# Optimization experiments

Measured on AMD Instinct MI355X. Metric: run time of the kernel, lower is better.

## Reference

```python
import jax, jax.numpy as jnp
import numpy as np

D_STATE = 16
DT_RANK = 6
EPS = 1e-5


def layer_norm(x, w, b):
    mu = jnp.mean(x, axis=-1, keepdims=True)
    var = jnp.mean((x - mu) ** 2, axis=-1, keepdims=True)
    return (x - mu) * jax.lax.rsqrt(var + EPS) * w + b


def selective_scan(u, delta, A, Bp, Cp, Dp):
    # u, delta: [B,L,D]; A: [D,N]; Bp, Cp: [B,L,N]; Dp: [D]
    delta_A = jnp.exp(jnp.einsum('bld,dn->bldn', delta, A))          # [B,L,D,N]
    delta_B_u = jnp.einsum('bld,bln,bld->bldn', delta, Bp, u)        # [B,L,D,N]
    Bsz, L, D = u.shape

    def step(x, inp):
        dA_t, dBu_t, C_t = inp                                       # [B,D,N],[B,D,N],[B,N]
        x = dA_t * x + dBu_t
        y = jnp.einsum('bdn,bn->bd', x, C_t)
        return x, y

    x0 = jnp.zeros((Bsz, D, D_STATE), dtype=u.dtype)
    xs = (jnp.swapaxes(delta_A, 0, 1), jnp.swapaxes(delta_B_u, 0, 1), jnp.swapaxes(Cp, 0, 1))
    _, ys = jax.lax.scan(step, x0, xs)                               # ys: [L,B,D]
    y = jnp.swapaxes(ys, 0, 1)
    return y + u * Dp


def ssm(x, x_proj_W, dt_proj_W, dt_proj_b, A_log, D_param):
    A = -jnp.exp(A_log.astype(jnp.float32))                         # [D,N]
    dbc = x @ x_proj_W.T                                             # [B,L,dt_rank+2N]
    delta_r = dbc[..., :DT_RANK]
    Bp = dbc[..., DT_RANK:DT_RANK + D_STATE]
    Cp = dbc[..., DT_RANK + D_STATE:]
    delta = jax.nn.softplus(delta_r @ dt_proj_W.T + dt_proj_b) * 0.001
    return selective_scan(x, delta, A, Bp, Cp, D_param.astype(jnp.float32))


def reference(feat_patch, ln_w, ln_b, in_proj_W, conv_w, conv_b,
              x_proj_W, dt_proj_W, dt_proj_b, A_log, D_param, out_proj_W):
    residual = feat_patch
    x = layer_norm(feat_patch, ln_w, ln_b)
    x = x @ in_proj_W.T                                              # [B,L,96]
    x_ncl = jnp.swapaxes(x, 1, 2)                                    # [B,96,L]
    x_ncl = jax.lax.conv_general_dilated(
        x_ncl, conv_w, window_strides=(1,), padding=((1, 1),),
        dimension_numbers=('NCH', 'OIH', 'NCH'), feature_group_count=96)
    x_ncl = x_ncl + conv_b[None, :, None]
    x = jnp.swapaxes(x_ncl, 1, 2)                                    # [B,L,96]
    x = jax.nn.silu(x)
    y = ssm(x, x_proj_W, dt_proj_W, dt_proj_b, A_log, D_param)
    out = y @ out_proj_W.T                                           # [B,L,2048]
    return out + residual


def setup_inputs() -> dict:
    key = jax.random.key(0)
    ks = jax.random.split(key, 10)
    B, L, C, Din = 16, 2048, 2048, 96
    A = jnp.tile(jnp.arange(1, D_STATE + 1, dtype=jnp.float32)[None, :], (Din, 1))
    return {
        'feat_patch': jax.random.normal(ks[0], (B, L, C), dtype=jnp.float32),
        'ln_w': jnp.ones((C,), jnp.float32),
        'ln_b': jnp.zeros((C,), jnp.float32),
        'in_proj_W': jax.random.normal(ks[1], (Din, C), jnp.float32) * (1.0 / np.sqrt(C)),
        'conv_w': jax.random.normal(ks[2], (Din, 1, 3), jnp.float32) * 0.3,
        'conv_b': jnp.zeros((Din,), jnp.float32),
        'x_proj_W': jax.random.normal(ks[3], (DT_RANK + 2 * D_STATE, Din), jnp.float32) * (1.0 / np.sqrt(Din)),
        'dt_proj_W': jax.random.normal(ks[4], (Din, DT_RANK), jnp.float32) * (1.0 / np.sqrt(DT_RANK)),
        'dt_proj_b': jnp.zeros((Din,), jnp.float32),
        'A_log': jnp.log(A),
        'D_param': jnp.ones((Din,), jnp.float32),
        'out_proj_W': jax.random.normal(ks[5], (C, Din), jnp.float32) * (1.0 / np.sqrt(Din)),
    }
```

## Files before the change

kernel.cpp:

```cpp
#include <hip/hip_runtime.h>
#include <hip/hip_bf16.h>

#define BSZ 16
#define LEN 2048
#define CH  2048
#define DIN 96
#define NST 16
#define RNK 6
#define NROW (BSZ*LEN)
#define TCH  256
#define NCHK (LEN/TCH)
#define NPAIR (BSZ*DIN)

typedef __attribute__((ext_vector_type(4))) float f32x4;
typedef __attribute__((ext_vector_type(8))) short bf16x8;

static __device__ __forceinline__ unsigned short f2bf(float f) {
  union { float f; unsigned u; } v; v.f = f;
  unsigned r = v.u + 0x7fff + ((v.u >> 16) & 1);
  return (unsigned short)(r >> 16);
}

static __device__ __forceinline__ f32x4 mfma16(bf16x8 a, bf16x8 b, f32x4 c) {
  return __builtin_amdgcn_mfma_f32_16x16x32_bf16(a, b, c, 0, 0, 0);
}

__global__ void k_prep(const float* __restrict__ inW, const float* __restrict__ outW,
                       const float* __restrict__ xW, const float* __restrict__ dtW,
                       const float* __restrict__ lnw,
                       unsigned short* __restrict__ inWb, unsigned short* __restrict__ outWb,
                       float* __restrict__ M1t, float* __restrict__ xBC) {
  int i = blockIdx.x * 256 + threadIdx.x;
  if (i < DIN*CH)  inWb[i]  = f2bf(inW[i] * lnw[i & (CH-1)]);
  if (i < CH*DIN)  outWb[i] = f2bf(outW[i]);
  if (i < DIN*DIN) {
    int c = i / DIN, d = i - c*DIN;
    float s = 0.f;
    #pragma unroll
    for (int r = 0; r < RNK; ++r) s += dtW[d*RNK + r] * xW[r*DIN + c];
    M1t[i] = s;
  }
  if (i < DIN*32) {
    int c = i / 32, n = i - c*32;
    xBC[i] = xW[(RNK + n)*DIN + c];
  }
}

__launch_bounds__(256)
__global__ void k_prep2(const float* __restrict__ inW, const float* __restrict__ lnw,
                        const float* __restrict__ lnb,
                        float* __restrict__ pvec, float* __restrict__ qvec) {
  __shared__ float sp_[4], sq_[4];
  const int d = blockIdx.x;
  const int tid = threadIdx.x;
  const float4* w4 = (const float4*)(inW + (size_t)d*CH);
  const float4* a4 = (const float4*)lnw;
  const float4* b4 = (const float4*)lnb;
  float sp = 0.f, sq = 0.f;
  for (int j = tid; j < CH/4; j += 256) {
    float4 w = w4[j], a = a4[j], b = b4[j];
    sp += w.x*a.x + w.y*a.y + w.z*a.z + w.w*a.w;
    sq += w.x*b.x + w.y*b.y + w.z*b.z + w.w*b.w;
  }
  #pragma unroll
  for (int off = 32; off; off >>= 1) { sp += __shfl_xor(sp, off); sq += __shfl_xor(sq, off); }
  if ((tid & 63) == 0) { sp_[tid>>6] = sp; sq_[tid>>6] = sq; }
  __syncthreads();
  if (tid == 0) {
    pvec[d] = sp_[0] + sp_[1] + sp_[2] + sp_[3];
    qvec[d] = sq_[0] + sq_[1] + sq_[2] + sq_[3];
  }
}

#define K2_KC 128
#define K2_WLD 136

__launch_bounds__(512)
__global__ void k_ln_inproj(const float* __restrict__ feat,
                            const unsigned short* __restrict__ Wb,
                            const float* __restrict__ pvec, const float* __restrict__ qvec,
                            float* __restrict__ xin) {
  __shared__ unsigned short W_lds[DIN][K2_WLD];

  const int tid  = threadIdx.x;
  const int lane = tid & 63;
  const int w    = tid >> 6;
  const int wh   = w & 3;
  const int wc   = w >> 2;
  const int r    = lane & 15;
  const int g    = lane >> 4;
  const int row  = blockIdx.x * 64 + wh*16 + r;

  const float* arow = feat + (size_t)row * CH;

  f32x4 acc[3];
  #pragma unroll
  for (int i = 0; i < 3; ++i) acc[i] = (f32x4){0.f, 0.f, 0.f, 0.f};
  float s = 0.f, q = 0.f;

  for (int kc = 0; kc < CH; kc += K2_KC) {
    __syncthreads();
    #pragma unroll
    for (int i = 0; i < 3; ++i) {
      int j = tid + 512*i;
      int wr = j >> 4, c16 = j & 15;
      *(uint4*)&W_lds[wr][c16*8] = *(const uint4*)(Wb + (size_t)wr*CH + kc + c16*8);
    }
    __syncthreads();
    #pragma unroll
    for (int t = 0; t < 4; ++t) {
      const float* ap = arow + kc + t*32 + g*8;
      float4 v0 = *(const float4*)ap;
      float4 v1 = *(const float4*)(ap + 4);
      s += v0.x + v0.y + v0.z + v0.w + v1.x + v1.y + v1.z + v1.w;
      q = fmaf(v0.x, v0.x, q); q = fmaf(v0.y, v0.y, q);
      q = fmaf(v0.z, v0.z, q); q = fmaf(v0.w, v0.w, q);
      q = fmaf(v1.x, v1.x, q); q = fmaf(v1.y, v1.y, q);
      q = fmaf(v1.z, v1.z, q); q = fmaf(v1.w, v1.w, q);
      union { bf16x8 v; unsigned short u[8]; } af;
      af.u[0] = f2bf(v0.x); af.u[1] = f2bf(v0.y); af.u[2] = f2bf(v0.z); af.u[3] = f2bf(v0.w);
      af.u[4] = f2bf(v1.x); af.u[5] = f2bf(v1.y); af.u[6] = f2bf(v1.z); af.u[7] = f2bf(v1.w);
      const int krd = t*32 + g*8;
      #pragma unroll
      for (int ct = 0; ct < 3; ++ct) {
        bf16x8 wf = *(const bf16x8*)&W_lds[wc*48 + ct*16 + r][krd];
        acc[ct] = mfma16(wf, af.v, acc[ct]);
      }
    }
  }

  s += __shfl_xor(s, 16); s += __shfl_xor(s, 32);
  q += __shfl_xor(q, 16); q += __shfl_xor(q, 32);
  const float mu = s * (1.f/CH);
  const float rs = rsqrtf(q*(1.f/CH) - mu*mu + 1e-5f);

  float* orow = xin + (size_t)row * DIN;
  #pragma unroll
  for (int ct = 0; ct < 3; ++ct) {
    const int col = wc*48 + ct*16 + g*4;
    float4 pv = *(const float4*)(pvec + col);
    float4 qv = *(const float4*)(qvec + col);
    f32x4 a = acc[ct];
    float4 o;
    o.x = rs*a[0] - rs*mu*pv.x + qv.x;
    o.y = rs*a[1] - rs*mu*pv.y + qv.y;
    o.z = rs*a[2] - rs*mu*pv.z + qv.z;
    o.w = rs*a[3] - rs*mu*pv.w + qv.w;
    *(float4*)(orow + col) = o;
  }
}

#define K3_R 8
__launch_bounds__(128)
__global__ void k_conv_proj(const float* __restrict__ xin,
                            const float* __restrict__ cw, const float* __restrict__ cb,
                            const float* __restrict__ xBC, const float* __restrict__ M1t,
                            const float* __restrict__ dtb,
                            float* __restrict__ ugT, float* __restrict__ dgT,
                            float* __restrict__ Bg, float* __restrict__ Cg) {
  __shared__ float su[K3_R][DIN];
  const int b  = blockIdx.y;
  const int l0 = blockIdx.x * K3_R;
  const int t  = threadIdx.x;

  if (t < DIN) {
    float x[K3_R + 2];
    #pragma unroll
    for (int i = 0; i < K3_R + 2; ++i) {
      int li = l0 - 1 + i;
      x[i] = (li >= 0 && li < LEN) ? xin[((size_t)b*LEN + li)*DIN + t] : 0.f;
    }
    float w0 = cw[t*3], w1 = cw[t*3+1], w2 = cw[t*3+2], bb = cb[t];
    float ua[K3_R];
    #pragma unroll
    for (int r = 0; r < K3_R; ++r) {
      float c = w0*x[r] + w1*x[r+1] + w2*x[r+2] + bb;
      float uu = c / (1.f + __expf(-c));
      su[r][t] = uu;
      ua[r] = uu;
    }
    float* up = ugT + ((size_t)(b*DIN + t))*LEN + l0;
    *(float4*)(up)     = make_float4(ua[0], ua[1], ua[2], ua[3]);
    *(float4*)(up + 4) = make_float4(ua[4], ua[5], ua[6], ua[7]);
  }
  __syncthreads();
  if (t < DIN) {
    float z[K3_R];
    #pragma unroll
    for (int r = 0; r < K3_R; ++r) z[r] = dtb[t];
    for (int c = 0; c < DIN; ++c) {
      float m = M1t[c*DIN + t];
      #pragma unroll
      for (int r = 0; r < K3_R; ++r) z[r] += su[r][c] * m;
    }
    float da[K3_R];
    #pragma unroll
    for (int r = 0; r < K3_R; ++r) {
      float zz = z[r];
      float sp = (zz > 20.f) ? zz : log1pf(__expf(zz));
      da[r] = 0.001f * sp;
    }
    float* dp = dgT + ((size_t)(b*DIN + t))*LEN + l0;
    *(float4*)(dp)     = make_float4(da[0], da[1], da[2], da[3]);
    *(float4*)(dp + 4) = make_float4(da[4], da[5], da[6], da[7]);
  } else if (t < DIN + 32) {
    int n = t - DIN;
    float s[K3_R];
    #pragma unroll
    for (int r = 0; r < K3_R; ++r) s[r] = 0.f;
    for (int c = 0; c < DIN; ++c) {
      float wv = xBC[c*32 + n];
      #pragma unroll
      for (int r = 0; r < K3_R; ++r) s[r] += su[r][c] * wv;
    }
    #pragma unroll
    for (int r = 0; r < K3_R; ++r) {
      size_t row = (size_t)b*LEN + l0 + r;
      if (n < 16) Bg[row*NST + n]        = s[r];
      else        Cg[row*NST + (n - 16)] = s[r];
    }
  }
}

__launch_bounds__(256)
__global__ void k_scan1(const float* __restrict__ dgT, const float* __restrict__ ugT,
                        const float* __restrict__ Bg, const float* __restrict__ Alog,
                        float* __restrict__ carryS, float* __restrict__ carryD) {
  const int tid  = threadIdx.x;
  const int n    = tid & 15;
  const int pair = blockIdx.x * 16 + (tid >> 4);
  const int chunk = blockIdx.y;
  const int b = pair / DIN, d = pair - b*DIN;
  const float An = -__expf(Alog[d*NST + n]);
  const float* dp  = dgT + ((size_t)(b*DIN + d))*LEN + chunk*TCH;
  const float* up  = ugT + ((size_t)(b*DIN + d))*LEN + chunk*TCH;
  const float* bp_ = Bg + ((size_t)b*LEN + chunk*TCH)*NST + n;

  float s = 0.f, sdl = 0.f;
  #pragma unroll 2
  for (int tq = 0; tq < TCH/4; ++tq) {
    f32x4 dl4 = *(const f32x4*)(dp + tq*4);
    f32x4 uu4 = *(const f32x4*)(up + tq*4);
    #pragma unroll
    for (int j = 0; j < 4; ++j) {
      float dl = dl4[j];
      float bp = bp_[(size_t)(tq*4 + j)*NST];
      s = fmaf(__expf(dl*An), s, dl*bp*uu4[j]);
      sdl += dl;
    }
  }
  carryS[(size_t)(pair*NCHK + chunk)*16 + n] = s;
  if (n == 0) carryD[pair*NCHK + chunk] = sdl;
}

__launch_bounds__(256)
__global__ void k_scan2(const float* __restrict__ carryS, const float* __restrict__ carryD,
                        const float* __restrict__ Alog, float* __restrict__ xstart) {
  const int i = blockIdx.x * 256 + threadIdx.x;
  const int pair = i >> 4, n = i & 15;
  const int d = pair % DIN;
  const float An = -__expf(Alog[d*NST + n]);
  float x = 0.f;
  #pragma unroll
  for (int c = 0; c < NCHK; ++c) {
    xstart[(size_t)(pair*NCHK + c)*16 + n] = x;
    x = fmaf(__expf(An * carryD[pair*NCHK + c]), x, carryS[(size_t)(pair*NCHK + c)*16 + n]);
  }
}

__launch_bounds__(256)
__global__ void k_scan3(const float* __restrict__ dgT, const float* __restrict__ ugT,
                        const float* __restrict__ Bg, const float* __restrict__ Cg,
                        const float* __restrict__ Alog, const float* __restrict__ Dp,
                        const float* __restrict__ xstart, unsigned short* __restrict__ yb) {
  const int tid  = threadIdx.x;
  const int n    = tid & 15;
  const int pair = blockIdx.x * 16 + (tid >> 4);
  const int chunk = blockIdx.y;
  const int b = pair / DIN, d = pair - b*DIN;
  const float An = -__expf(Alog[d*NST + n]);
  const float Dd = Dp[d];
  const float* dp  = dgT + ((size_t)(b*DIN + d))*LEN + chunk*TCH;
  const float* up  = ugT + ((size_t)(b*DIN + d))*LEN + chunk*TCH;
  const float* bp_ = Bg + ((size_t)b*LEN + chunk*TCH)*NST + n;
  const float* cp_ = Cg + ((size_t)b*LEN + chunk*TCH)*NST + n;
  unsigned short* yp = yb + ((size_t)b*LEN + chunk*TCH)*DIN + d;

  float s = xstart[(size_t)(pair*NCHK + chunk)*16 + n];
  #pragma unroll 2
  for (int tq = 0; tq < TCH/4; ++tq) {
    f32x4 dl4 = *(const f32x4*)(dp + tq*4);
    f32x4 uu4 = *(const f32x4*)(up + tq*4);
    #pragma unroll
    for (int j = 0; j < 4; ++j) {
      float dl = dl4[j];
      float bp = bp_[(size_t)(tq*4 + j)*NST];
      float cp = cp_[(size_t)(tq*4 + j)*NST];
      s = fmaf(__expf(dl*An), s, dl*bp*uu4[j]);
      float py = s * cp;
      py += __shfl_xor(py, 8);
      py += __shfl_xor(py, 4);
      py += __shfl_xor(py, 2);
      py += __shfl_xor(py, 1);
      if (n == 0) yp[(size_t)(tq*4 + j)*DIN] = f2bf(py + uu4[j]*Dd);
    }
  }
}

#define K6_MR 128
#define K6_NC 128
#define K6_LD 104

__launch_bounds__(512)
__global__ void k_outproj(const unsigned short* __restrict__ yb,
                          const unsigned short* __restrict__ Wb,
                          const float* __restrict__ resid,
                          float* __restrict__ out) {
  __shared__ unsigned short W_lds[K6_NC][K6_LD];
  const int tid  = threadIdx.x;
  const int lane = tid & 63;
  const int w    = tid >> 6;
  const int r    = lane & 15;
  const int g    = lane >> 4;
  const int r0   = blockIdx.y * K6_MR;
  const int c0   = blockIdx.x * K6_NC;

  #pragma unroll
  for (int i = 0; i < 3; ++i) {
    int j = tid + 512*i;
    int row = j / 12, c8 = j - row*12;
    *(uint4*)&W_lds[row][c8*8] = *(const uint4*)(Wb + (size_t)(c0 + row)*DIN + c8*8);
  }
  __syncthreads();

  f32x4 acc[8];
  #pragma unroll
  for (int i = 0; i < 8; ++i) acc[i] = (f32x4){0.f, 0.f, 0.f, 0.f};

  const unsigned short* yrow = yb + (size_t)(r0 + w*16 + r)*DIN;
  #pragma unroll
  for (int kt = 0; kt < 3; ++kt) {
    const int krd = kt*32 + g*8;
    bf16x8 y0 = *(const bf16x8*)(yrow + krd);
    #pragma unroll
    for (int ci = 0; ci < 8; ++ci) {
      bf16x8 wf = *(const bf16x8*)&W_lds[ci*16 + r][krd];
      acc[ci] = mfma16(wf, y0, acc[ci]);
    }
  }

  const size_t row = (size_t)(r0 + w*16 + r);
  #pragma unroll
  for (int ci = 0; ci < 8; ++ci) {
    size_t col = (size_t)(c0 + ci*16 + g*4);
    const f32x4 rv = *(const f32x4*)(resid + row*CH + col);
    f32x4 o = acc[ci] + rv;
    __builtin_nontemporal_store(o, (f32x4*)(out + row*CH + col));
  }
}

extern "C" void kernel_launch(void* const* d_in, const int* in_sizes, int n_in,
                              void* d_out, int out_size, void* d_ws, size_t ws_size,
                              hipStream_t stream) {
  const float* feat = (const float*)d_in[0];
  const float* lnw  = (const float*)d_in[1];
  const float* lnb  = (const float*)d_in[2];
  const float* inW  = (const float*)d_in[3];
  const float* cw   = (const float*)d_in[4];
  const float* cb   = (const float*)d_in[5];
  const float* xW   = (const float*)d_in[6];
  const float* dtW  = (const float*)d_in[7];
  const float* dtb  = (const float*)d_in[8];
  const float* Alog = (const float*)d_in[9];
  const float* Dp   = (const float*)d_in[10];
  const float* outW = (const float*)d_in[11];
  float* out = (float*)d_out;

  char* ws = (char*)d_ws;
  size_t off = 0;
  auto alloc = [&](size_t bytes) { void* p = ws + off; off += (bytes + 255) & ~255ull; return p; };
  unsigned short* inWb  = (unsigned short*)alloc((size_t)DIN*CH*2);
  unsigned short* outWb = (unsigned short*)alloc((size_t)CH*DIN*2);
  float* M1t = (float*)alloc((size_t)DIN*DIN*4);
  float* xBC = (float*)alloc((size_t)DIN*32*4);
  float* pvec = (float*)alloc((size_t)DIN*4);
  float* qvec = (float*)alloc((size_t)DIN*4);
  float* xin = (float*)alloc((size_t)NROW*DIN*4);
  float* ugT = (float*)alloc((size_t)NROW*DIN*4);
  float* dgT = (float*)alloc((size_t)NROW*DIN*4);
  float* Bg  = (float*)alloc((size_t)NROW*NST*4);
  float* Cg  = (float*)alloc((size_t)NROW*NST*4);
  unsigned short* yb = (unsigned short*)alloc((size_t)NROW*DIN*2);
  float* carryS = (float*)alloc((size_t)NPAIR*NCHK*NST*4);
  float* carryD = (float*)alloc((size_t)NPAIR*NCHK*4);
  float* xstart = (float*)alloc((size_t)NPAIR*NCHK*NST*4);

  hipLaunchKernelGGL(k_prep, dim3((DIN*CH + 255)/256), dim3(256), 0, stream,
                     inW, outW, xW, dtW, lnw, inWb, outWb, M1t, xBC);
  hipLaunchKernelGGL(k_prep2, dim3(DIN), dim3(256), 0, stream,
                     inW, lnw, lnb, pvec, qvec);
  hipLaunchKernelGGL(k_ln_inproj, dim3(NROW/64), dim3(512), 0, stream,
                     feat, inWb, pvec, qvec, xin);
  hipLaunchKernelGGL(k_conv_proj, dim3(LEN/K3_R, BSZ), dim3(128), 0, stream,
                     xin, cw, cb, xBC, M1t, dtb, ugT, dgT, Bg, Cg);
  hipLaunchKernelGGL(k_scan1, dim3(NPAIR/16, NCHK), dim3(256), 0, stream,
                     dgT, ugT, Bg, Alog, carryS, carryD);
  hipLaunchKernelGGL(k_scan2, dim3(NPAIR*NST/256), dim3(256), 0, stream,
                     carryS, carryD, Alog, xstart);
  hipLaunchKernelGGL(k_scan3, dim3(NPAIR/16, NCHK), dim3(256), 0, stream,
                     dgT, ugT, Bg, Cg, Alog, Dp, xstart, yb);
  hipLaunchKernelGGL(k_outproj, dim3(CH/K6_NC, NROW/K6_MR), dim3(512), 0, stream,
                     yb, outWb, feat, out);
}
```

Measured before the change: 378.4 us.

## Process four scan states per thread and halve scan chunk length

The scan kernels now assign four SSM states per thread using vector loads of B/C/A, replacing sixteen lanes per channel pair. This cuts the shuffle reduction from four steps to two and allows wider memory accesses. The chunk length is halved to keep enough blocks in flight now that each block covers more pairs. The large feature and residual streams are also read with nontemporal loads to reduce cache pollution. The trade-off is more per-thread register pressure and serial exp work per step.

Measured after the change: 357.8 us. -5.4%, faster.

```diff
diff --git a/kernel.cpp b/kernel.cpp
--- a/kernel.cpp
+++ b/kernel.cpp
@@ -8,7 +8,7 @@
 #define NST 16
 #define RNK 6
 #define NROW (BSZ*LEN)
-#define TCH  256
+#define TCH  128
 #define NCHK (LEN/TCH)
 #define NPAIR (BSZ*DIN)
 
@@ -109,17 +109,15 @@
     __syncthreads();
     #pragma unroll
     for (int t = 0; t < 4; ++t) {
-      const float* ap = arow + kc + t*32 + g*8;
-      float4 v0 = *(const float4*)ap;
-      float4 v1 = *(const float4*)(ap + 4);
-      s += v0.x + v0.y + v0.z + v0.w + v1.x + v1.y + v1.z + v1.w;
-      q = fmaf(v0.x, v0.x, q); q = fmaf(v0.y, v0.y, q);
-      q = fmaf(v0.z, v0.z, q); q = fmaf(v0.w, v0.w, q);
-      q = fmaf(v1.x, v1.x, q); q = fmaf(v1.y, v1.y, q);
-      q = fmaf(v1.z, v1.z, q); q = fmaf(v1.w, v1.w, q);
+      const f32x4* ap = (const f32x4*)(arow + kc + t*32 + g*8);
+      f32x4 v0 = __builtin_nontemporal_load(ap);
+      f32x4 v1 = __builtin_nontemporal_load(ap + 1);
+      s += v0[0] + v0[1] + v0[2] + v0[3] + v1[0] + v1[1] + v1[2] + v1[3];
+      #pragma unroll
+      for (int k = 0; k < 4; ++k) { q = fmaf(v0[k], v0[k], q); q = fmaf(v1[k], v1[k], q); }
       union { bf16x8 v; unsigned short u[8]; } af;
-      af.u[0] = f2bf(v0.x); af.u[1] = f2bf(v0.y); af.u[2] = f2bf(v0.z); af.u[3] = f2bf(v0.w);
-      af.u[4] = f2bf(v1.x); af.u[5] = f2bf(v1.y); af.u[6] = f2bf(v1.z); af.u[7] = f2bf(v1.w);
+      #pragma unroll
+      for (int k = 0; k < 4; ++k) { af.u[k] = f2bf(v0[k]); af.u[4+k] = f2bf(v1[k]); }
       const int krd = t*32 + g*8;
       #pragma unroll
       for (int ct = 0; ct < 3; ++ct) {
@@ -227,16 +225,20 @@
                         const float* __restrict__ Bg, const float* __restrict__ Alog,
                         float* __restrict__ carryS, float* __restrict__ carryD) {
   const int tid  = threadIdx.x;
-  const int n    = tid & 15;
-  const int pair = blockIdx.x * 16 + (tid >> 4);
+  const int nq   = tid & 3;
+  const int pair = blockIdx.x * 64 + (tid >> 2);
   const int chunk = blockIdx.y;
   const int b = pair / DIN, d = pair - b*DIN;
-  const float An = -__expf(Alog[d*NST + n]);
+  f32x4 Al = *(const f32x4*)(Alog + d*NST + nq*4);
+  f32x4 An4;
+  #pragma unroll
+  for (int k = 0; k < 4; ++k) An4[k] = -__expf(Al[k]);
   const float* dp  = dgT + ((size_t)(b*DIN + d))*LEN + chunk*TCH;
   const float* up  = ugT + ((size_t)(b*DIN + d))*LEN + chunk*TCH;
-  const float* bp_ = Bg + ((size_t)b*LEN + chunk*TCH)*NST + n;
-
-  float s = 0.f, sdl = 0.f;
+  const float* bp_ = Bg + ((size_t)b*LEN + chunk*TCH)*NST + nq*4;
+
+  f32x4 s4 = (f32x4){0.f, 0.f, 0.f, 0.f};
+  float sdl = 0.f;
   #pragma unroll 2
   for (int tq = 0; tq < TCH/4; ++tq) {
     f32x4 dl4 = *(const f32x4*)(dp + tq*4);
@@ -244,13 +246,17 @@
     #pragma unroll
     for (int j = 0; j < 4; ++j) {
       float dl = dl4[j];
-      float bp = bp_[(size_t)(tq*4 + j)*NST];
-      s = fmaf(__expf(dl*An), s, dl*bp*uu4[j]);
+      f32x4 bp4 = *(const f32x4*)(bp_ + (size_t)(tq*4 + j)*NST);
+      f32x4 dA;
+      #pragma unroll
+      for (int k = 0; k < 4; ++k) dA[k] = __expf(dl*An4[k]);
+      float du = dl * uu4[j];
+      s4 = dA*s4 + du*bp4;
       sdl += dl;
     }
   }
-  carryS[(size_t)(pair*NCHK + chunk)*16 + n] = s;
-  if (n == 0) carryD[pair*NCHK + chunk] = sdl;
+  *(f32x4*)(carryS + (size_t)(pair*NCHK + chunk)*16 + nq*4) = s4;
+  if (nq == 0) carryD[pair*NCHK + chunk] = sdl;
 }
 
 __launch_bounds__(256)
@@ -274,19 +280,22 @@
                         const float* __restrict__ Alog, const float* __restrict__ Dp,
                         const float* __restrict__ xstart, unsigned short* __restrict__ yb) {
   const int tid  = threadIdx.x;
-  const int n    = tid & 15;
-  const int pair = blockIdx.x * 16 + (tid >> 4);
+  const int nq   = tid & 3;
+  const int pair = blockIdx.x * 64 + (tid >> 2);
   const int chunk = blockIdx.y;
   const int b = pair / DIN, d = pair - b*DIN;
-  const float An = -__expf(Alog[d*NST + n]);
+  f32x4 Al = *(const f32x4*)(Alog + d*NST + nq*4);
+  f32x4 An4;
+  #pragma unroll
+  for (int k = 0; k < 4; ++k) An4[k] = -__expf(Al[k]);
   const float Dd = Dp[d];
   const float* dp  = dgT + ((size_t)(b*DIN + d))*LEN + chunk*TCH;
   const float* up  = ugT + ((size_t)(b*DIN + d))*LEN + chunk*TCH;
-  const float* bp_ = Bg + ((size_t)b*LEN + chunk*TCH)*NST + n;
-  const float* cp_ = Cg + ((size_t)b*LEN + chunk*TCH)*NST + n;
+  const float* bp_ = Bg + ((size_t)b*LEN + chunk*TCH)*NST + nq*4;
+  const float* cp_ = Cg + ((size_t)b*LEN + chunk*TCH)*NST + nq*4;
   unsigned short* yp = yb + ((size_t)b*LEN + chunk*TCH)*DIN + d;
 
-  float s = xstart[(size_t)(pair*NCHK + chunk)*16 + n];
+  f32x4 s4 = *(const f32x4*)(xstart + (size_t)(pair*NCHK + chunk)*16 + nq*4);
   #pragma unroll 2
   for (int tq = 0; tq < TCH/4; ++tq) {
     f32x4 dl4 = *(const f32x4*)(dp + tq*4);
@@ -294,15 +303,18 @@
     #pragma unroll
     for (int j = 0; j < 4; ++j) {
       float dl = dl4[j];
-      float bp = bp_[(size_t)(tq*4 + j)*NST];
-      float cp = cp_[(size_t)(tq*4 + j)*NST];
-      s = fmaf(__expf(dl*An), s, dl*bp*uu4[j]);
-      float py = s * cp;
-      py += __shfl_xor(py, 8);
-      py += __shfl_xor(py, 4);
+      f32x4 bp4 = *(const f32x4*)(bp_ + (size_t)(tq*4 + j)*NST);
+      f32x4 cp4 = *(const f32x4*)(cp_ + (size_t)(tq*4 + j)*NST);
+      f32x4 dA;
+      #pragma unroll
+      for (int k = 0; k < 4; ++k) dA[k] = __expf(dl*An4[k]);
+      float du = dl * uu4[j];
+      s4 = dA*s4 + du*bp4;
+      f32x4 pv = s4 * cp4;
+      float py = (pv[0] + pv[1]) + (pv[2] + pv[3]);
+      py += __shfl_xor(py, 1);
       py += __shfl_xor(py, 2);
-      py += __shfl_xor(py, 1);
-      if (n == 0) yp[(size_t)(tq*4 + j)*DIN] = f2bf(py + uu4[j]*Dd);
+      if (nq == 0) yp[(size_t)(tq*4 + j)*DIN] = f2bf(py + uu4[j]*Dd);
     }
   }
 }
@@ -353,7 +365,7 @@
   #pragma unroll
   for (int ci = 0; ci < 8; ++ci) {
     size_t col = (size_t)(c0 + ci*16 + g*4);
-    const f32x4 rv = *(const f32x4*)(resid + row*CH + col);
+    const f32x4 rv = __builtin_nontemporal_load((const f32x4*)(resid + row*CH + col));
     f32x4 o = acc[ci] + rv;
     __builtin_nontemporal_store(o, (f32x4*)(out + row*CH + col));
   }
@@ -403,11 +415,11 @@
                      feat, inWb, pvec, qvec, xin);
   hipLaunchKernelGGL(k_conv_proj, dim3(LEN/K3_R, BSZ), dim3(128), 0, stream,
                      xin, cw, cb, xBC, M1t, dtb, ugT, dgT, Bg, Cg);
-  hipLaunchKernelGGL(k_scan1, dim3(NPAIR/16, NCHK), dim3(256), 0, stream,
+  hipLaunchKernelGGL(k_scan1, dim3(NPAIR/64, NCHK), dim3(256), 0, stream,
                      dgT, ugT, Bg, Alog, carryS, carryD);
   hipLaunchKernelGGL(k_scan2, dim3(NPAIR*NST/256), dim3(256), 0, stream,
                      carryS, carryD, Alog, xstart);
-  hipLaunchKernelGGL(k_scan3, dim3(NPAIR/16, NCHK), dim3(256), 0, stream,
+  hipLaunchKernelGGL(k_scan3, dim3(NPAIR/64, NCHK), dim3(256), 0, stream,
                      dgT, ugT, Bg, Cg, Alog, Dp, xstart, yb);
   hipLaunchKernelGGL(k_outproj, dim3(CH/K6_NC, NROW/K6_MR), dim3(512), 0, stream,
                      yb, outWb, feat, out);
```
